# Optimization experiments

Measured on AMD Instinct MI355X. Metric: run time of the kernel, lower is better.

## Reference

```python
import jax, jax.numpy as jnp
import numpy as np

V = 780        # junction-tree vocab size
N = 50000      # total nodes in batch
M = 100001     # total messages (+1 null slot at index 0)
K = 6          # padded max neighbors
H = 256        # hidden size
B = 64         # number of trees (scope entries)
DEPTH = 6      # GRU depth


def setup_inputs() -> dict:
    key = jax.random.key(0)
    ks = jax.random.split(key, 12)
    p = lambda k, s: jax.random.normal(k, s, jnp.float32) * 0.02
    return {
        "fnode": jax.random.randint(ks[0], (N,), 0, V),
        "fmess": jax.random.randint(ks[1], (M,), 0, N),
        "node_graph": jax.random.randint(ks[2], (N, K), 0, M),
        "mess_graph": jax.random.randint(ks[3], (M, K), 0, M),
        "scope_st": jax.random.randint(ks[4], (B,), 0, N),
        "emb": p(ks[5], (V, H)),
        "Wz": p(ks[6], (H, 2 * H)), "bz": jnp.zeros((H,), jnp.float32),
        "Wr": p(ks[7], (H, H)),
        "Ur": p(ks[8], (H, H)), "bu": jnp.zeros((H,), jnp.float32),
        "Wh": p(ks[9], (H, 2 * H)), "bh": jnp.zeros((H,), jnp.float32),
        "Wo": p(ks[10], (H, 2 * H)), "bo": jnp.zeros((H,), jnp.float32),
    }


def reference(fnode, fmess, node_graph, mess_graph, scope_st,
              emb, Wz, bz, Wr, Ur, bu, Wh, bh, Wo, bo):
    fnode_e = emb[fnode]                       # [N, H] embedded node features
    x = fnode_e[fmess]                         # [M, H] per-message source features
    mask = jnp.ones((M, 1), jnp.float32).at[0].set(0.0)  # zero the null message
    # W_r(x) depends only on x; hoist it out of the loop (same math as original)
    xWr = (x @ Wr.T)[:, None, :]               # [M, 1, H]

    h = jnp.zeros((M, H), jnp.float32)
    for _ in range(DEPTH):
        h_nei = h[mess_graph]                  # [M, K, H] gather neighbor messages
        sum_h = h_nei.sum(axis=1)              # [M, H]
        z = jax.nn.sigmoid(jnp.concatenate([x, sum_h], axis=1) @ Wz.T + bz)
        r = jax.nn.sigmoid(xWr + h_nei @ Ur.T + bu)   # [M, K, H]
        sum_gated_h = (r * h_nei).sum(axis=1)  # [M, H]
        pre_h = jnp.tanh(jnp.concatenate([x, sum_gated_h], axis=1) @ Wh.T + bh)
        h = ((1.0 - z) * sum_h + z * pre_h) * mask

    mess_nei = h[node_graph].sum(axis=1)       # [N, H]
    node_vecs = jax.nn.relu(
        jnp.concatenate([fnode_e, mess_nei], axis=-1) @ Wo.T + bo)  # [N, H]
    tree_vecs = node_vecs[scope_st]            # [B, H] root vector per tree
    return tree_vecs, h
```

## Files before the change

kernel.cpp:

```cpp
#include <hip/hip_runtime.h>

typedef unsigned short u16;
typedef unsigned int   u32;
typedef short bf16x8 __attribute__((ext_vector_type(8)));
typedef float f32x4  __attribute__((ext_vector_type(4)));

#define V_ 780
#define N_ 50000
#define M_ 100001
#define K_ 6
#define H_ 256
#define B_ 64
#define DEPTH_ 6

#define HE_LD 512

typedef __attribute__((address_space(3))) u32 lds_u32;
typedef __attribute__((address_space(1))) const u32 glb_u32;
__device__ __forceinline__ void dma16(const void* g, void* l){
  __builtin_amdgcn_global_load_lds((glb_u32*)g, (lds_u32*)l, 16, 0, 0);
}

__device__ __forceinline__ float b2f(u16 u){
  union { u32 i; float f; } x; x.i = ((u32)u) << 16; return x.f;
}
__device__ __forceinline__ u16 f2b(float f){
  union { float f; u32 i; } x; x.f = f;
  u32 r = x.i + 0x7fffu + ((x.i >> 16) & 1u);
  return (u16)(r >> 16);
}
__device__ __forceinline__ float rcp_(float x){ return __builtin_amdgcn_rcpf(x); }
__device__ __forceinline__ float sigm(float x){ return rcp_(1.f + __expf(-x)); }
__device__ __forceinline__ float tanh_(float x){
  x = fminf(fmaxf(x, -15.f), 15.f);
  float e = __expf(2.f*x);
  return (e - 1.f) * rcp_(e + 1.f);
}
__device__ __forceinline__ int swz(int r){ return (r + (r >> 2)) & 3; }

__global__ void k_tables(const float* __restrict__ emb,
    const float* __restrict__ Wz, const float* __restrict__ bz,
    const float* __restrict__ Wr, const float* __restrict__ bu,
    const float* __restrict__ Wh, const float* __restrict__ bh,
    const float* __restrict__ Wo, const float* __restrict__ bo,
    float* __restrict__ tWz, float* __restrict__ tXr,
    float* __restrict__ tWh, float* __restrict__ tWo){
  int v = blockIdx.x, q = blockIdx.y, j = threadIdx.x;
  __shared__ float e[H_];
  e[j] = emb[v*H_ + j];
  __syncthreads();
  const float* w; const float* b; float* o; int ld;
  if      (q == 0){ w = Wz; b = bz; o = tWz; ld = 2*H_; }
  else if (q == 1){ w = Wr; b = bu; o = tXr; ld = H_;   }
  else if (q == 2){ w = Wh; b = bh; o = tWh; ld = 2*H_; }
  else            { w = Wo; b = bo; o = tWo; ld = 2*H_; }
  const float* wr = w + (size_t)j*ld;
  float a0 = 0.f, a1 = 0.f;
  #pragma unroll 4
  for (int i = 0; i < H_; i += 8){
    float4 x = *(const float4*)(wr + i);
    float4 y = *(const float4*)(wr + i + 4);
    a0 += e[i  ]*x.x + e[i+1]*x.y + e[i+2]*x.z + e[i+3]*x.w;
    a1 += e[i+4]*y.x + e[i+5]*y.y + e[i+6]*y.z + e[i+7]*y.w;
  }
  float val = a0 + a1 + b[j];
  if (q == 1) val = __expf(-val);
  o[v*H_ + j] = val;
}

__global__ void k_convw(const float* __restrict__ Ur, const float* __restrict__ Wz,
                        const float* __restrict__ Wh,
                        u16* __restrict__ Urb, u16* __restrict__ Wzb, u16* __restrict__ Whb){
  int r = blockIdx.x, j = threadIdx.x;
  Urb[r*H_ + j] = f2b(Ur[r*H_ + j]);
  Wzb[r*H_ + j] = f2b(Wz[r*(2*H_) + H_ + j]);
  Whb[r*H_ + j] = f2b(Wh[r*(2*H_) + H_ + j]);
}

__global__ void k_init(const int* __restrict__ fnode, const int* __restrict__ fmess,
                       const float* __restrict__ tWz, const float* __restrict__ tWh,
                       int* __restrict__ vmsg, u16* __restrict__ hE){
  int m = blockIdx.x, j = threadIdx.x;
  int v = fnode[fmess[m]];
  if (j == 0) vmsg[m] = v;
  float val = (m == 0) ? 0.f : sigm(tWz[v*H_ + j])*tanh_(tWh[v*H_ + j]);
  hE[(size_t)m*HE_LD + j] = f2b(val);
}

__global__ void k_gather(const u16* __restrict__ hE,
                         const int* __restrict__ mg, const int* __restrict__ vmsg,
                         const float* __restrict__ tXr,
                         u16* __restrict__ sumh, u16* __restrict__ sumg){
  int m = blockIdx.x*4 + (threadIdx.x >> 6);
  if (m >= M_) return;
  const int lane = threadIdx.x & 63;
  int v = vmsg[m];
  float4 X = *(const float4*)(tXr + (size_t)v*H_ + lane*4);
  const int2* mgp = (const int2*)(mg + m*K_);
  int2 g01 = mgp[0], g23 = mgp[1], g45 = mgp[2];
  int gs[K_] = {g01.x, g01.y, g23.x, g23.y, g45.x, g45.y};
  const char* bc = (const char*)hE;
  const u32 cb = (u32)lane * 8u;
  float s0=0.f,s1=0.f,s2=0.f,s3=0.f, a0=0.f,a1=0.f,a2=0.f,a3=0.f;
  #pragma unroll
  for (int k=0;k<K_;k++){
    u32 off = ((u32)gs[k] << 10) + cb;
    uint2 hp = *(const uint2*)(bc + off);
    uint2 ep = *(const uint2*)(bc + off + 512);
    float h0=b2f((u16)hp.x), h1=b2f((u16)(hp.x>>16));
    float h2=b2f((u16)hp.y), h3=b2f((u16)(hp.y>>16));
    float e0=b2f((u16)ep.x), e1=b2f((u16)(ep.x>>16));
    float e2=b2f((u16)ep.y), e3=b2f((u16)(ep.y>>16));
    s0+=h0; s1+=h1; s2+=h2; s3+=h3;
    a0 += rcp_(fmaf(X.x,e0,1.f))*h0;
    a1 += rcp_(fmaf(X.y,e1,1.f))*h1;
    a2 += rcp_(fmaf(X.z,e2,1.f))*h2;
    a3 += rcp_(fmaf(X.w,e3,1.f))*h3;
  }
  uint2 sh, sg;
  sh.x = (u32)f2b(s0) | ((u32)f2b(s1)<<16);
  sh.y = (u32)f2b(s2) | ((u32)f2b(s3)<<16);
  sg.x = (u32)f2b(a0) | ((u32)f2b(a1)<<16);
  sg.y = (u32)f2b(a2) | ((u32)f2b(a3)<<16);
  *(uint2*)((char*)sumh + ((size_t)m<<9) + cb) = sh;
  *(uint2*)((char*)sumg + ((size_t)m<<9) + cb) = sg;
}

__global__ __launch_bounds__(256,3) void k_gemm(
    const u16* A, const u16* __restrict__ W, u16* C){
  __shared__ __align__(16) u16 lA[2][64*32];
  __shared__ __align__(16) u16 lB[2][256*32];
  const int t    = threadIdx.x;
  const int m0   = blockIdx.x * 64;
  const int lane = t & 63, wave = t >> 6;
  const int l16  = lane & 15, kc8 = lane >> 4;

  const int rA = t >> 2, cA = t & 3;
  const int kA = (cA ^ swz(rA)) * 8;
  const int gmA = (m0 + rA < M_) ? (m0 + rA) : (M_ - 1);
  const int aOff = (wave*64)*8;
  int rB[4], kB[4], bOff[4];
  #pragma unroll
  for (int p=0;p<4;p++){
    int s = t + 256*p;
    rB[p] = s >> 2; int cc = s & 3;
    kB[p] = (cc ^ swz(rB[p])) * 8;
    bOff[p] = (wave*64 + 256*p)*8;
  }

  f32x4 acc[4][4];
  #pragma unroll
  for (int r=0;r<4;r++)
    #pragma unroll
    for (int c=0;c<4;c++)
      #pragma unroll
      for (int q=0;q<4;q++) acc[r][c][q] = 0.f;

  auto stage = [&](int buf, int k0){
    dma16(A + (size_t)gmA*HE_LD + k0 + kA, &lA[buf][aOff]);
    #pragma unroll
    for (int p=0;p<4;p++)
      dma16(W + (size_t)rB[p]*H_ + k0 + kB[p], &lB[buf][bOff[p]]);
  };

  stage(0, 0);
  __syncthreads();
  int cur = 0;
  for (int ks = 0; ks < 8; ++ks){
    if (ks < 7) stage(cur^1, (ks+1)*32);
    bf16x8 aF[4], bF[4];
    #pragma unroll
    for (int r=0;r<4;r++){
      int row = r*16 + l16;
      aF[r] = *(const bf16x8*)(&lA[cur][row*32 + ((kc8 ^ swz(row))*8)]);
    }
    #pragma unroll
    for (int c=0;c<4;c++){
      int row = wave*64 + c*16 + l16;
      bF[c] = *(const bf16x8*)(&lB[cur][row*32 + ((kc8 ^ swz(row))*8)]);
    }
    #pragma unroll
    for (int r=0;r<4;r++)
      #pragma unroll
      for (int c=0;c<4;c++)
        acc[r][c] = __builtin_amdgcn_mfma_f32_16x16x32_bf16(aF[r], bF[c], acc[r][c], 0,0,0);
    if (ks < 7) __syncthreads();
    cur ^= 1;
  }

  #pragma unroll
  for (int r=0;r<4;r++){
    #pragma unroll
    for (int c=0;c<4;c++){
      int mb = m0 + r*16 + kc8*4;
      int n  = wave*64 + c*16 + l16;
      #pragma unroll
      for (int q=0;q<4;q++){
        int m = mb + q;
        if (m < M_) C[(size_t)m*HE_LD + H_ + n] = f2b(__expf(-acc[r][c][q]));
      }
    }
  }
}

template<bool F32OUT>
__global__ __launch_bounds__(256,3) void k_gemmzh(
    const u16* __restrict__ sumh, const u16* __restrict__ sumg,
    const u16* __restrict__ Wzb, const u16* __restrict__ Whb,
    void* __restrict__ Cv,
    const float* __restrict__ tWz, const float* __restrict__ tWh,
    const int* __restrict__ vmsg){
  __shared__ __align__(16) u16 lH[2][64*32];
  __shared__ __align__(16) u16 lG[2][64*32];
  __shared__ __align__(16) u16 lZ[2][128*32];
  __shared__ __align__(16) u16 lW[2][128*32];
  const int t    = threadIdx.x;
  const int m0   = (blockIdx.x >> 1) * 64;
  const int n0   = (blockIdx.x & 1) * 128;
  const int lane = t & 63, wave = t >> 6;
  const int wrow = wave >> 1, wcol = wave & 1;
  const int l16  = lane & 15, kc8 = lane >> 4;

  const int rA = t >> 2, cA = t & 3;
  const int kA = (cA ^ swz(rA)) * 8;
  const int gmA = (m0 + rA < M_) ? (m0 + rA) : (M_ - 1);
  const int aOff = (wave*64)*8;
  int rB[2], kB[2], bOff[2];
  #pragma unroll
  for (int p=0;p<2;p++){
    int s = t + 256*p;
    rB[p] = s >> 2; int cc = s & 3;
    kB[p] = (cc ^ swz(rB[p])) * 8;
    bOff[p] = (wave*64 + 256*p)*8;
  }

  f32x4 accZ[2][4], accH[2][4];
  #pragma unroll
  for (int r=0;r<2;r++)
    #pragma unroll
    for (int c=0;c<4;c++)
      #pragma unroll
      for (int q=0;q<4;q++){ accZ[r][c][q] = 0.f; accH[r][c][q] = 0.f; }

  auto stage = [&](int buf, int k0){
    dma16(sumh + (size_t)gmA*H_ + k0 + kA, &lH[buf][aOff]);
    dma16(sumg + (size_t)gmA*H_ + k0 + kA, &lG[buf][aOff]);
    #pragma unroll
    for (int p=0;p<2;p++){
      dma16(Wzb + (size_t)(n0+rB[p])*H_ + k0 + kB[p], &lZ[buf][bOff[p]]);
      dma16(Whb + (size_t)(n0+rB[p])*H_ + k0 + kB[p], &lW[buf][bOff[p]]);
    }
  };

  stage(0, 0);
  __syncthreads();
  int cur = 0;
  for (int ks = 0; ks < 8; ++ks){
    if (ks < 7) stage(cur^1, (ks+1)*32);
    bf16x8 aH[2], aG[2];
    #pragma unroll
    for (int r=0;r<2;r++){
      int row = wrow*32 + r*16 + l16;
      int off = row*32 + ((kc8 ^ swz(row))*8);
      aH[r] = *(const bf16x8*)(&lH[cur][off]);
      aG[r] = *(const bf16x8*)(&lG[cur][off]);
    }
    #pragma unroll
    for (int c=0;c<4;c++){
      int row = wcol*64 + c*16 + l16;
      int off = row*32 + ((kc8 ^ swz(row))*8);
      bf16x8 bZ = *(const bf16x8*)(&lZ[cur][off]);
      bf16x8 bW = *(const bf16x8*)(&lW[cur][off]);
      #pragma unroll
      for (int r=0;r<2;r++){
        accZ[r][c] = __builtin_amdgcn_mfma_f32_16x16x32_bf16(aH[r], bZ, accZ[r][c], 0,0,0);
        accH[r][c] = __builtin_amdgcn_mfma_f32_16x16x32_bf16(aG[r], bW, accH[r][c], 0,0,0);
      }
    }
    if (ks < 7) __syncthreads();
    cur ^= 1;
  }

  #pragma unroll
  for (int r=0;r<2;r++){
    #pragma unroll
    for (int q=0;q<4;q++){
      int m = m0 + wrow*32 + r*16 + kc8*4 + q;
      if (m >= M_) continue;
      int v = vmsg[m];
      #pragma unroll
      for (int c=0;c<4;c++){
        int n = n0 + wcol*64 + c*16 + l16;
        float z   = sigm(tWz[v*H_ + n] + accZ[r][c][q]);
        float pre = tanh_(tWh[v*H_ + n] + accH[r][c][q]);
        float sh  = b2f(sumh[(size_t)m*H_ + n]);
        float o   = (m == 0) ? 0.f : (1.f - z)*sh + z*pre;
        if (F32OUT) ((float*)Cv)[(size_t)m*H_ + n] = o;
        else        ((u16*)Cv)[(size_t)m*HE_LD + n] = f2b(o);
      }
    }
  }
}

__global__ void k_final(const float* __restrict__ h, const int* __restrict__ ng,
                        const int* __restrict__ fnode, const int* __restrict__ scope,
                        const float* __restrict__ tWo, const float* __restrict__ Wo,
                        float* __restrict__ out){
  int b = blockIdx.x, j = threadIdx.x;
  int n = scope[b];
  __shared__ float mn[H_];
  float s = 0.f;
  #pragma unroll
  for (int k=0;k<K_;k++){
    int g = ng[n*K_ + k];
    s += h[(size_t)g*H_ + j];
  }
  mn[j] = s;
  __syncthreads();
  int v = fnode[n];
  float acc = tWo[v*H_ + j];
  const float* w = Wo + j*(2*H_) + H_;
  for (int i=0;i<H_;i+=4){
    float4 a = *(const float4*)(w+i);
    acc += mn[i]*a.x + mn[i+1]*a.y + mn[i+2]*a.z + mn[i+3]*a.w;
  }
  out[b*H_ + j] = fmaxf(acc, 0.f);
}

__global__ void k_zero(float* __restrict__ out, int n){
  int i = blockIdx.x*256 + threadIdx.x;
  int stride = gridDim.x*256;
  for (; i < n; i += stride) out[i] = 0.f;
}

extern "C" void kernel_launch(void* const* d_in, const int* in_sizes, int n_in,
                              void* d_out, int out_size, void* d_ws, size_t ws_size,
                              hipStream_t stream){
  const int* fnode      = (const int*)d_in[0];
  const int* fmess      = (const int*)d_in[1];
  const int* node_graph = (const int*)d_in[2];
  const int* mess_graph = (const int*)d_in[3];
  const int* scope_st   = (const int*)d_in[4];
  const float* emb = (const float*)d_in[5];
  const float* Wz  = (const float*)d_in[6];
  const float* bz  = (const float*)d_in[7];
  const float* Wr  = (const float*)d_in[8];
  const float* Ur  = (const float*)d_in[9];
  const float* bu  = (const float*)d_in[10];
  const float* Wh  = (const float*)d_in[11];
  const float* bh  = (const float*)d_in[12];
  const float* Wo  = (const float*)d_in[13];
  const float* bo  = (const float*)d_in[14];

  char* ws = (char*)d_ws;
  size_t off = 0;
  float* tWz = (float*)(ws + off); off += (size_t)V_*H_*4;
  float* tXr = (float*)(ws + off); off += (size_t)V_*H_*4;
  float* tWh = (float*)(ws + off); off += (size_t)V_*H_*4;
  float* tWo = (float*)(ws + off); off += (size_t)V_*H_*4;
  u16* Urb  = (u16*)(ws + off); off += (size_t)H_*H_*2;
  u16* Wzb  = (u16*)(ws + off); off += (size_t)H_*H_*2;
  u16* Whb  = (u16*)(ws + off); off += (size_t)H_*H_*2;
  int* vmsg = (int*)(ws + off); off += ((size_t)M_*4 + 511) & ~(size_t)511;
  u16* sumh = (u16*)(ws + off); off += (size_t)M_*H_*2;
  u16* sumg = (u16*)(ws + off); off += (size_t)M_*H_*2;

  if (ws_size < off){
    k_zero<<<2048, 256, 0, stream>>>((float*)d_out, out_size);
    return;
  }

  float* out = (float*)d_out;
  float* h   = out + (size_t)B_*H_;
  u16* hE = (u16*)h;

  const int MT64 = (M_ + 63)/64;
  const int GG   = 2*MT64;

  k_tables<<<dim3(V_,4), H_, 0, stream>>>(emb, Wz, bz, Wr, bu, Wh, bh, Wo, bo,
                                          tWz, tXr, tWh, tWo);
  k_convw<<<H_, H_, 0, stream>>>(Ur, Wz, Wh, Urb, Wzb, Whb);
  k_init<<<M_, H_, 0, stream>>>(fnode, fmess, tWz, tWh, vmsg, hE);

  for (int it = 0; it < DEPTH_-1; ++it){
    k_gemm<<<MT64, 256, 0, stream>>>(hE, Urb, hE);
    k_gather<<<(M_+3)/4, 256, 0, stream>>>(hE, mess_graph, vmsg, tXr, sumh, sumg);
    if (it < DEPTH_-2)
      k_gemmzh<false><<<GG, 256, 0, stream>>>(sumh, sumg, Wzb, Whb, hE,
                                              tWz, tWh, vmsg);
    else
      k_gemmzh<true ><<<GG, 256, 0, stream>>>(sumh, sumg, Wzb, Whb, h,
                                              tWz, tWh, vmsg);
  }

  k_final<<<B_, H_, 0, stream>>>(h, node_graph, fnode, scope_st, tWo, Wo, out);
}
```

Baseline: 1.361 ms.

## Fuse gather, gate GEMMs and next Ur GEMM into one per-step kernel

Replaces the per-iteration gather, z/h GEMM and Ur GEMM kernels with a single k_step kernel. Each block gathers neighbor sums for 64 messages straight into swizzled LDS, runs the Wz/Wh MFMAs, applies the GRU update, then reuses the new h tile in LDS to compute the next iteration's exp(-Ur·h) half. This removes the sumh/sumg global round-trips and two launches per step. Because blocks now read neighbors while others write, ping-pong buffers (workspace and output) are used. Weight operands are read directly from global memory rather than staged in LDS, and occupancy falls with 64KB of LDS per block.

```diff
diff --git a/kernel.cpp b/kernel.cpp
--- a/kernel.cpp
+++ b/kernel.cpp
@@ -37,6 +37,9 @@
   return (e - 1.f) * rcp_(e + 1.f);
 }
 __device__ __forceinline__ int swz(int r){ return (r + (r >> 2)) & 3; }
+__device__ __forceinline__ int lds_off(int row, int col){
+  return row*256 + ((((col >> 3) ^ (row & 7)) << 3) + (col & 7));
+}
 
 __global__ void k_tables(const float* __restrict__ emb,
     const float* __restrict__ Wz, const float* __restrict__ bz,
@@ -87,45 +90,6 @@
   hE[(size_t)m*HE_LD + j] = f2b(val);
 }
 
-__global__ void k_gather(const u16* __restrict__ hE,
-                         const int* __restrict__ mg, const int* __restrict__ vmsg,
-                         const float* __restrict__ tXr,
-                         u16* __restrict__ sumh, u16* __restrict__ sumg){
-  int m = blockIdx.x*4 + (threadIdx.x >> 6);
-  if (m >= M_) return;
-  const int lane = threadIdx.x & 63;
-  int v = vmsg[m];
-  float4 X = *(const float4*)(tXr + (size_t)v*H_ + lane*4);
-  const int2* mgp = (const int2*)(mg + m*K_);
-  int2 g01 = mgp[0], g23 = mgp[1], g45 = mgp[2];
-  int gs[K_] = {g01.x, g01.y, g23.x, g23.y, g45.x, g45.y};
-  const char* bc = (const char*)hE;
-  const u32 cb = (u32)lane * 8u;
-  float s0=0.f,s1=0.f,s2=0.f,s3=0.f, a0=0.f,a1=0.f,a2=0.f,a3=0.f;
-  #pragma unroll
-  for (int k=0;k<K_;k++){
-    u32 off = ((u32)gs[k] << 10) + cb;
-    uint2 hp = *(const uint2*)(bc + off);
-    uint2 ep = *(const uint2*)(bc + off + 512);
-    float h0=b2f((u16)hp.x), h1=b2f((u16)(hp.x>>16));
-    float h2=b2f((u16)hp.y), h3=b2f((u16)(hp.y>>16));
-    float e0=b2f((u16)ep.x), e1=b2f((u16)(ep.x>>16));
-    float e2=b2f((u16)ep.y), e3=b2f((u16)(ep.y>>16));
-    s0+=h0; s1+=h1; s2+=h2; s3+=h3;
-    a0 += rcp_(fmaf(X.x,e0,1.f))*h0;
-    a1 += rcp_(fmaf(X.y,e1,1.f))*h1;
-    a2 += rcp_(fmaf(X.z,e2,1.f))*h2;
-    a3 += rcp_(fmaf(X.w,e3,1.f))*h3;
-  }
-  uint2 sh, sg;
-  sh.x = (u32)f2b(s0) | ((u32)f2b(s1)<<16);
-  sh.y = (u32)f2b(s2) | ((u32)f2b(s3)<<16);
-  sg.x = (u32)f2b(a0) | ((u32)f2b(a1)<<16);
-  sg.y = (u32)f2b(a2) | ((u32)f2b(a3)<<16);
-  *(uint2*)((char*)sumh + ((size_t)m<<9) + cb) = sh;
-  *(uint2*)((char*)sumg + ((size_t)m<<9) + cb) = sg;
-}
-
 __global__ __launch_bounds__(256,3) void k_gemm(
     const u16* A, const u16* __restrict__ W, u16* C){
   __shared__ __align__(16) u16 lA[2][64*32];
@@ -203,36 +167,62 @@
   }
 }
 
-template<bool F32OUT>
-__global__ __launch_bounds__(256,3) void k_gemmzh(
-    const u16* __restrict__ sumh, const u16* __restrict__ sumg,
+template<bool FIN>
+__global__ __launch_bounds__(512,4) void k_step(
+    const u16* __restrict__ src, u16* __restrict__ dst,
+    float* __restrict__ hf,
+    const int* __restrict__ mg, const int* __restrict__ vmsg,
+    const float* __restrict__ tXr, const float* __restrict__ tWz,
+    const float* __restrict__ tWh,
     const u16* __restrict__ Wzb, const u16* __restrict__ Whb,
-    void* __restrict__ Cv,
-    const float* __restrict__ tWz, const float* __restrict__ tWh,
-    const int* __restrict__ vmsg){
-  __shared__ __align__(16) u16 lH[2][64*32];
-  __shared__ __align__(16) u16 lG[2][64*32];
-  __shared__ __align__(16) u16 lZ[2][128*32];
-  __shared__ __align__(16) u16 lW[2][128*32];
+    const u16* __restrict__ Urb){
+  __shared__ __align__(16) u16 lSH[64*256];
+  __shared__ __align__(16) u16 lSG[64*256];
   const int t    = threadIdx.x;
-  const int m0   = (blockIdx.x >> 1) * 64;
-  const int n0   = (blockIdx.x & 1) * 128;
+  const int m0   = blockIdx.x * 64;
   const int lane = t & 63, wave = t >> 6;
-  const int wrow = wave >> 1, wcol = wave & 1;
   const int l16  = lane & 15, kc8 = lane >> 4;
-
-  const int rA = t >> 2, cA = t & 3;
-  const int kA = (cA ^ swz(rA)) * 8;
-  const int gmA = (m0 + rA < M_) ? (m0 + rA) : (M_ - 1);
-  const int aOff = (wave*64)*8;
-  int rB[2], kB[2], bOff[2];
-  #pragma unroll
-  for (int p=0;p<2;p++){
-    int s = t + 256*p;
-    rB[p] = s >> 2; int cc = s & 3;
-    kB[p] = (cc ^ swz(rB[p])) * 8;
-    bOff[p] = (wave*64 + 256*p)*8;
-  }
+  const int wrow = wave >> 2, wcol = wave & 3;
+
+  {
+    const char* bc = (const char*)src;
+    const u32 cb = (u32)lane * 8u;
+    #pragma unroll 2
+    for (int i = 0; i < 8; ++i){
+      int row = wave*8 + i;
+      int gm = m0 + row; if (gm >= M_) gm = M_ - 1;
+      int v = vmsg[gm];
+      float4 X = *(const float4*)(tXr + (size_t)v*H_ + lane*4);
+      const int2* mgp = (const int2*)(mg + gm*K_);
+      int2 g01 = mgp[0], g23 = mgp[1], g45 = mgp[2];
+      int gs[K_] = {g01.x,g01.y,g23.x,g23.y,g45.x,g45.y};
+      float s0=0.f,s1=0.f,s2=0.f,s3=0.f, a0=0.f,a1=0.f,a2=0.f,a3=0.f;
+      #pragma unroll
+      for (int k=0;k<K_;k++){
+        u32 off = ((u32)gs[k] << 10) + cb;
+        uint2 hp = *(const uint2*)(bc + off);
+        uint2 ep = *(const uint2*)(bc + off + 512);
+        float h0=b2f((u16)hp.x), h1=b2f((u16)(hp.x>>16));
+        float h2=b2f((u16)hp.y), h3=b2f((u16)(hp.y>>16));
+        float e0=b2f((u16)ep.x), e1=b2f((u16)(ep.x>>16));
+        float e2=b2f((u16)ep.y), e3=b2f((u16)(ep.y>>16));
+        s0+=h0; s1+=h1; s2+=h2; s3+=h3;
+        a0 += rcp_(fmaf(X.x,e0,1.f))*h0;
+        a1 += rcp_(fmaf(X.y,e1,1.f))*h1;
+        a2 += rcp_(fmaf(X.z,e2,1.f))*h2;
+        a3 += rcp_(fmaf(X.w,e3,1.f))*h3;
+      }
+      uint2 sh, sg;
+      sh.x = (u32)f2b(s0) | ((u32)f2b(s1)<<16);
+      sh.y = (u32)f2b(s2) | ((u32)f2b(s3)<<16);
+      sg.x = (u32)f2b(a0) | ((u32)f2b(a1)<<16);
+      sg.y = (u32)f2b(a2) | ((u32)f2b(a3)<<16);
+      int o = lds_off(row, lane*4);
+      *(uint2*)&lSH[o] = sh;
+      *(uint2*)&lSG[o] = sg;
+    }
+  }
+  __syncthreads();
 
   f32x4 accZ[2][4], accH[2][4];
   #pragma unroll
@@ -240,63 +230,96 @@
     #pragma unroll
     for (int c=0;c<4;c++)
       #pragma unroll
-      for (int q=0;q<4;q++){ accZ[r][c][q] = 0.f; accH[r][c][q] = 0.f; }
-
-  auto stage = [&](int buf, int k0){
-    dma16(sumh + (size_t)gmA*H_ + k0 + kA, &lH[buf][aOff]);
-    dma16(sumg + (size_t)gmA*H_ + k0 + kA, &lG[buf][aOff]);
-    #pragma unroll
-    for (int p=0;p<2;p++){
-      dma16(Wzb + (size_t)(n0+rB[p])*H_ + k0 + kB[p], &lZ[buf][bOff[p]]);
-      dma16(Whb + (size_t)(n0+rB[p])*H_ + k0 + kB[p], &lW[buf][bOff[p]]);
-    }
-  };
-
-  stage(0, 0);
-  __syncthreads();
-  int cur = 0;
-  for (int ks = 0; ks < 8; ++ks){
-    if (ks < 7) stage(cur^1, (ks+1)*32);
+      for (int q=0;q<4;q++){ accZ[r][c][q]=0.f; accH[r][c][q]=0.f; }
+
+  #pragma unroll
+  for (int ks=0; ks<8; ++ks){
     bf16x8 aH[2], aG[2];
     #pragma unroll
     for (int r=0;r<2;r++){
       int row = wrow*32 + r*16 + l16;
-      int off = row*32 + ((kc8 ^ swz(row))*8);
-      aH[r] = *(const bf16x8*)(&lH[cur][off]);
-      aG[r] = *(const bf16x8*)(&lG[cur][off]);
+      int o = row*256 + ((((ks*4 + kc8) ^ (row & 7)) << 3));
+      aH[r] = *(const bf16x8*)&lSH[o];
+      aG[r] = *(const bf16x8*)&lSG[o];
     }
     #pragma unroll
     for (int c=0;c<4;c++){
-      int row = wcol*64 + c*16 + l16;
-      int off = row*32 + ((kc8 ^ swz(row))*8);
-      bf16x8 bZ = *(const bf16x8*)(&lZ[cur][off]);
-      bf16x8 bW = *(const bf16x8*)(&lW[cur][off]);
+      int n = wcol*64 + c*16 + l16;
+      bf16x8 bZ = *(const bf16x8*)(Wzb + (size_t)n*H_ + ks*32 + kc8*8);
+      bf16x8 bW = *(const bf16x8*)(Whb + (size_t)n*H_ + ks*32 + kc8*8);
       #pragma unroll
       for (int r=0;r<2;r++){
         accZ[r][c] = __builtin_amdgcn_mfma_f32_16x16x32_bf16(aH[r], bZ, accZ[r][c], 0,0,0);
         accH[r][c] = __builtin_amdgcn_mfma_f32_16x16x32_bf16(aG[r], bW, accH[r][c], 0,0,0);
       }
     }
-    if (ks < 7) __syncthreads();
-    cur ^= 1;
-  }
-
+  }
+  __syncthreads();
+
+  #pragma unroll
+  for (int r=0;r<2;r++){
+    #pragma unroll
+    for (int q=0;q<4;q++){
+      int lm = wrow*32 + r*16 + kc8*4 + q;
+      int m  = m0 + lm;
+      int v  = (m < M_) ? vmsg[m] : 0;
+      #pragma unroll
+      for (int c=0;c<4;c++){
+        int n = wcol*64 + c*16 + l16;
+        float z   = sigm(tWz[v*H_ + n] + accZ[r][c][q]);
+        float pre = tanh_(tWh[v*H_ + n] + accH[r][c][q]);
+        float sh  = b2f(lSH[lds_off(lm, n)]);
+        float o   = (m == 0) ? 0.f : (1.f - z)*sh + z*pre;
+        if (FIN){
+          if (m < M_) hf[(size_t)m*H_ + n] = o;
+        } else {
+          u16 ob = f2b(o);
+          if (m < M_) dst[(size_t)m*HE_LD + n] = ob;
+          lSG[lds_off(lm, n)] = ob;
+        }
+      }
+    }
+  }
+
+  if (FIN) return;
+  __syncthreads();
+
+  f32x4 accE[2][4];
+  #pragma unroll
+  for (int r=0;r<2;r++)
+    #pragma unroll
+    for (int c=0;c<4;c++)
+      #pragma unroll
+      for (int q=0;q<4;q++) accE[r][c][q] = 0.f;
+
+  #pragma unroll
+  for (int ks=0; ks<8; ++ks){
+    bf16x8 aN[2];
+    #pragma unroll
+    for (int r=0;r<2;r++){
+      int row = wrow*32 + r*16 + l16;
+      int o = row*256 + ((((ks*4 + kc8) ^ (row & 7)) << 3));
+      aN[r] = *(const bf16x8*)&lSG[o];
+    }
+    #pragma unroll
+    for (int c=0;c<4;c++){
+      int n = wcol*64 + c*16 + l16;
+      bf16x8 bU = *(const bf16x8*)(Urb + (size_t)n*H_ + ks*32 + kc8*8);
+      #pragma unroll
+      for (int r=0;r<2;r++)
+        accE[r][c] = __builtin_amdgcn_mfma_f32_16x16x32_bf16(aN[r], bU, accE[r][c], 0,0,0);
+    }
+  }
   #pragma unroll
   for (int r=0;r<2;r++){
     #pragma unroll
     for (int q=0;q<4;q++){
       int m = m0 + wrow*32 + r*16 + kc8*4 + q;
       if (m >= M_) continue;
-      int v = vmsg[m];
       #pragma unroll
       for (int c=0;c<4;c++){
-        int n = n0 + wcol*64 + c*16 + l16;
-        float z   = sigm(tWz[v*H_ + n] + accZ[r][c][q]);
-        float pre = tanh_(tWh[v*H_ + n] + accH[r][c][q]);
-        float sh  = b2f(sumh[(size_t)m*H_ + n]);
-        float o   = (m == 0) ? 0.f : (1.f - z)*sh + z*pre;
-        if (F32OUT) ((float*)Cv)[(size_t)m*H_ + n] = o;
-        else        ((u16*)Cv)[(size_t)m*HE_LD + n] = f2b(o);
+        int n = wcol*64 + c*16 + l16;
+        dst[(size_t)m*HE_LD + H_ + n] = f2b(__expf(-accE[r][c][q]));
       }
     }
   }
@@ -361,9 +384,8 @@
   u16* Urb  = (u16*)(ws + off); off += (size_t)H_*H_*2;
   u16* Wzb  = (u16*)(ws + off); off += (size_t)H_*H_*2;
   u16* Whb  = (u16*)(ws + off); off += (size_t)H_*H_*2;
-  int* vmsg = (int*)(ws + off); off += ((size_t)M_*4 + 511) & ~(size_t)511;
-  u16* sumh = (u16*)(ws + off); off += (size_t)M_*H_*2;
-  u16* sumg = (u16*)(ws + off); off += (size_t)M_*H_*2;
+  int* vmsg = (int*)(ws + off); off += ((size_t)M_*4 + 1023) & ~(size_t)1023;
+  u16* hEws = (u16*)(ws + off); off += (size_t)M_*HE_LD*2;
 
   if (ws_size < off){
     k_zero<<<2048, 256, 0, stream>>>((float*)d_out, out_size);
@@ -372,26 +394,26 @@
 
   float* out = (float*)d_out;
   float* h   = out + (size_t)B_*H_;
-  u16* hE = (u16*)h;
+  u16* hED = (u16*)h;
 
   const int MT64 = (M_ + 63)/64;
-  const int GG   = 2*MT64;
 
   k_tables<<<dim3(V_,4), H_, 0, stream>>>(emb, Wz, bz, Wr, bu, Wh, bh, Wo, bo,
                                           tWz, tXr, tWh, tWo);
   k_convw<<<H_, H_, 0, stream>>>(Ur, Wz, Wh, Urb, Wzb, Whb);
-  k_init<<<M_, H_, 0, stream>>>(fnode, fmess, tWz, tWh, vmsg, hE);
-
-  for (int it = 0; it < DEPTH_-1; ++it){
-    k_gemm<<<MT64, 256, 0, stream>>>(hE, Urb, hE);
-    k_gather<<<(M_+3)/4, 256, 0, stream>>>(hE, mess_graph, vmsg, tXr, sumh, sumg);
-    if (it < DEPTH_-2)
-      k_gemmzh<false><<<GG, 256, 0, stream>>>(sumh, sumg, Wzb, Whb, hE,
-                                              tWz, tWh, vmsg);
-    else
-      k_gemmzh<true ><<<GG, 256, 0, stream>>>(sumh, sumg, Wzb, Whb, h,
-                                              tWz, tWh, vmsg);
-  }
+  k_init<<<M_, H_, 0, stream>>>(fnode, fmess, tWz, tWh, vmsg, hEws);
+  k_gemm<<<MT64, 256, 0, stream>>>(hEws, Urb, hEws);
+
+  k_step<false><<<MT64, 512, 0, stream>>>(hEws, hED,  h, mess_graph, vmsg,
+                                          tXr, tWz, tWh, Wzb, Whb, Urb);
+  k_step<false><<<MT64, 512, 0, stream>>>(hED,  hEws, h, mess_graph, vmsg,
+                                          tXr, tWz, tWh, Wzb, Whb, Urb);
+  k_step<false><<<MT64, 512, 0, stream>>>(hEws, hED,  h, mess_graph, vmsg,
+                                          tXr, tWz, tWh, Wzb, Whb, Urb);
+  k_step<false><<<MT64, 512, 0, stream>>>(hED,  hEws, h, mess_graph, vmsg,
+                                          tXr, tWz, tWh, Wzb, Whb, Urb);
+  k_step<true ><<<MT64, 512, 0, stream>>>(hEws, hEws, h, mess_graph, vmsg,
+                                          tXr, tWz, tWh, Wzb, Whb, Urb);
 
   k_final<<<B_, H_, 0, stream>>>(h, node_graph, fnode, scope_st, tWo, Wo, out);
 }
```

Measured after the change: 1.546 ms. 13.6% more time.
